# Optimization experiments

Hardware: AMD Instinct MI355X
Metric: run time of the kernel (lower is better)

The kernel has to match this reference:

```python
import jax, jax.numpy as jnp
import numpy as np

EMBED_DIM = 1024
NUM_HEADS = 16
HEAD_DIM = EMBED_DIM // NUM_HEADS
B, S = 2, 2048


def setup_inputs() -> dict:
    key = jax.random.key(0)
    ks = jax.random.split(key, 11)
    sc = 1.0 / np.sqrt(EMBED_DIM)
    d = {
        'query': jax.random.normal(ks[0], (B, S, EMBED_DIM), jnp.float32),
        'key': jax.random.normal(ks[1], (B, S, EMBED_DIM), jnp.float32),
        'value': jax.random.normal(ks[2], (B, S, EMBED_DIM), jnp.float32),
        'Wq': jax.random.normal(ks[3], (EMBED_DIM, EMBED_DIM), jnp.float32) * sc,
        'bq': jnp.zeros((EMBED_DIM,), jnp.float32),
        'Wk': jax.random.normal(ks[4], (EMBED_DIM, EMBED_DIM), jnp.float32) * sc,
        'bk': jnp.zeros((EMBED_DIM,), jnp.float32),
        'Wv': jax.random.normal(ks[5], (EMBED_DIM, EMBED_DIM), jnp.float32) * sc,
        'bv': jnp.zeros((EMBED_DIM,), jnp.float32),
        'Wo': jax.random.normal(ks[6], (EMBED_DIM, EMBED_DIM), jnp.float32) * sc,
        'bo': jnp.zeros((EMBED_DIM,), jnp.float32),
    }
    return d


def reference(query, key, value, Wq, bq, Wk, bk, Wv, bv, Wo, bo):
    b, s, _ = query.shape
    scale = 1.0 / np.sqrt(HEAD_DIM)
    # projections: torch Linear is x @ W.T + b
    q = (query @ Wq.T + bq).reshape(b, s, NUM_HEADS, HEAD_DIM).transpose(0, 2, 1, 3)
    k = (key @ Wk.T + bk).reshape(b, s, NUM_HEADS, HEAD_DIM).transpose(0, 2, 1, 3)
    v = (value @ Wv.T + bv).reshape(b, s, NUM_HEADS, HEAD_DIM).transpose(0, 2, 1, 3)
    scores = jnp.einsum('bhqd,bhkd->bhqk', q, k) * scale  # [B,H,S,S]
    causal = jnp.triu(jnp.ones((s, s), bool), k=1)
    scores = jnp.where(causal, -jnp.inf, scores)
    attn = jax.nn.softmax(scores, axis=-1)
    out = jnp.einsum('bhqk,bhkd->bhqd', attn, v)
    out = out.transpose(0, 2, 1, 3).reshape(b, s, EMBED_DIM)
    out = out @ Wo.T + bo
    return out, attn
```

## Files before the change

kernel.cpp:

```cpp
#include <hip/hip_runtime.h>
#include <hip/hip_bf16.h>

#define BATCH  2
#define SEQ    2048
#define EMBED  1024
#define NHEADS 16
#define HDIM   64
#define SCALE  0.125f
#define S2     0.180336880f
#define MFIX   20.0f
#define PPITCH 72

typedef __attribute__((ext_vector_type(8))) short   short8;
typedef __attribute__((ext_vector_type(4))) float   floatx4;

#if __has_builtin(__builtin_amdgcn_exp2f)
#define EXP2(x) __builtin_amdgcn_exp2f(x)
#else
#define EXP2(x) exp2f(x)
#endif

#define GLOAD_LDS(g, l) __builtin_amdgcn_global_load_lds(                      \
    (const __attribute__((address_space(1))) void*)(const void*)(g),           \
    (__attribute__((address_space(3))) void*)(void*)(l), 16, 0, 0)

__device__ __forceinline__ float bf2f(unsigned short h) {
    union { unsigned int u; float f; } v; v.u = ((unsigned int)h) << 16; return v.f;
}
__device__ __forceinline__ unsigned short f2bf(float f) {
    union { float f; unsigned int u; } v; v.f = f;
    unsigned int r = v.u + 0x7FFF + ((v.u >> 16) & 1);
    return (unsigned short)(r >> 16);
}
__device__ __forceinline__ unsigned int pack2(float lo, float hi) {
    return (unsigned int)f2bf(lo) | ((unsigned int)f2bf(hi) << 16);
}

__device__ __forceinline__ void bar_lds() {
    __builtin_amdgcn_sched_barrier(0);
    asm volatile("s_waitcnt lgkmcnt(0)" ::: "memory");
    __builtin_amdgcn_s_barrier();
    __builtin_amdgcn_sched_barrier(0);
}

__global__ __launch_bounds__(256)
void cvt_bf16(const float* __restrict__ q,  const float* __restrict__ k,
              const float* __restrict__ v,  const float* __restrict__ wq,
              const float* __restrict__ wk, const float* __restrict__ wv,
              const float* __restrict__ wo,
              unsigned short* __restrict__ dq,  unsigned short* __restrict__ dk,
              unsigned short* __restrict__ dv,  unsigned short* __restrict__ dwq,
              unsigned short* __restrict__ dwk, unsigned short* __restrict__ dwv,
              unsigned short* __restrict__ dwo)
{
    const float* s; unsigned short* d; int n;
    switch (blockIdx.y) {
        case 0: s = q;  d = dq;  n = BATCH * SEQ * EMBED; break;
        case 1: s = k;  d = dk;  n = BATCH * SEQ * EMBED; break;
        case 2: s = v;  d = dv;  n = BATCH * SEQ * EMBED; break;
        case 3: s = wq; d = dwq; n = EMBED * EMBED; break;
        case 4: s = wk; d = dwk; n = EMBED * EMBED; break;
        case 5: s = wv; d = dwv; n = EMBED * EMBED; break;
        default: s = wo; d = dwo; n = EMBED * EMBED; break;
    }
    const int i = (blockIdx.x * 256 + threadIdx.x) * 8;
    if (i >= n) return;
    float4 f0 = ((const float4*)(s + i))[0];
    float4 f1 = ((const float4*)(s + i))[1];
    uint4 u = {pack2(f0.x, f0.y), pack2(f0.z, f0.w),
               pack2(f1.x, f1.y), pack2(f1.z, f1.w)};
    *(uint4*)(d + i) = u;
}

__device__ __forceinline__ void gemm_body(
    const unsigned short* __restrict__ A,
    const unsigned short* __restrict__ W,
    const float* __restrict__ bias,
    void* __restrict__ Cout, const int f32out,
    const int bx, const int by)
{
    constexpr int N = EMBED;
    constexpr int K = EMBED;

    __shared__ unsigned short As[128 * 64];
    __shared__ unsigned short Bs[128 * 64];

    const int t    = threadIdx.x;
    const int w    = t >> 6;
    const int lane = t & 63;
    const int lr   = lane & 15;
    const int quad = lane >> 4;
    const int wr   = w >> 1;
    const int wc   = w & 1;
    const int n0   = bx * 128;
    const int m0   = by * 128;

    size_t agoff[4], bgoff[4];
    #pragma unroll
    for (int i = 0; i < 4; ++i) {
        const int slot = i * 256 + t;
        const int row  = slot >> 3;
        const int g    = (slot & 7) ^ (row & 7);
        agoff[i] = (size_t)(m0 + row) * K + g * 8;
        bgoff[i] = (size_t)(n0 + row) * K + g * 8;
    }

    int aoff[4][2], boff[4][2];
    #pragma unroll
    for (int mb = 0; mb < 4; ++mb)
        #pragma unroll
        for (int s = 0; s < 2; ++s) {
            const int row = wr * 64 + mb * 16 + lr;
            aoff[mb][s] = row * 64 + (((s * 4 + quad) ^ (row & 7)) * 8);
        }
    #pragma unroll
    for (int nb = 0; nb < 4; ++nb)
        #pragma unroll
        for (int s = 0; s < 2; ++s) {
            const int row = wc * 64 + nb * 16 + lr;
            boff[nb][s] = row * 64 + (((s * 4 + quad) ^ (row & 7)) * 8);
        }

    floatx4 acc[4][4];
    #pragma unroll
    for (int mb = 0; mb < 4; ++mb)
        #pragma unroll
        for (int nb = 0; nb < 4; ++nb) acc[mb][nb] = (floatx4){0.f, 0.f, 0.f, 0.f};

    for (int k0 = 0; k0 < K; k0 += 64) {
        __syncthreads();
        #pragma unroll
        for (int i = 0; i < 4; ++i)
            GLOAD_LDS(A + agoff[i] + k0, &As[(i * 256 + w * 64) * 8]);
        #pragma unroll
        for (int i = 0; i < 4; ++i)
            GLOAD_LDS(W + bgoff[i] + k0, &Bs[(i * 256 + w * 64) * 8]);
        __syncthreads();

        #pragma unroll
        for (int s = 0; s < 2; ++s) {
            short8 av[4], bv[4];
            #pragma unroll
            for (int mb = 0; mb < 4; ++mb) av[mb] = *(const short8*)&As[aoff[mb][s]];
            #pragma unroll
            for (int nb = 0; nb < 4; ++nb) bv[nb] = *(const short8*)&Bs[boff[nb][s]];
            #pragma unroll
            for (int mb = 0; mb < 4; ++mb)
                #pragma unroll
                for (int nb = 0; nb < 4; ++nb)
                    acc[mb][nb] = __builtin_amdgcn_mfma_f32_16x16x32_bf16(av[mb], bv[nb], acc[mb][nb], 0, 0, 0);
        }
    }

    #pragma unroll
    for (int mb = 0; mb < 4; ++mb)
        #pragma unroll
        for (int nb = 0; nb < 4; ++nb) {
            const int col = n0 + wc * 64 + nb * 16 + lr;
            const float bv = bias[col];
            #pragma unroll
            for (int r = 0; r < 4; ++r) {
                const int row = m0 + wr * 64 + mb * 16 + quad * 4 + r;
                const float val = acc[mb][nb][r] + bv;
                if (f32out) ((float*)Cout)[(size_t)row * N + col] = val;
                else        ((unsigned short*)Cout)[(size_t)row * N + col] = f2bf(val);
            }
        }
}

__global__ __launch_bounds__(256)
void gemm_qkv(const unsigned short* __restrict__ xq, const unsigned short* __restrict__ xk,
              const unsigned short* __restrict__ xv,
              const unsigned short* __restrict__ wq, const unsigned short* __restrict__ wk,
              const unsigned short* __restrict__ wv,
              const float* __restrict__ bq, const float* __restrict__ bk,
              const float* __restrict__ bv,
              unsigned short* __restrict__ Qb, unsigned short* __restrict__ Kb,
              unsigned short* __restrict__ Vb)
{
    const unsigned short *A, *W; const float* bias; unsigned short* C;
    switch (blockIdx.z) {
        case 0:  A = xq; W = wq; bias = bq; C = Qb; break;
        case 1:  A = xk; W = wk; bias = bk; C = Kb; break;
        default: A = xv; W = wv; bias = bv; C = Vb; break;
    }
    gemm_body(A, W, bias, C, 0, blockIdx.x, blockIdx.y);
}

__global__ __launch_bounds__(256)
void gemm_out(const unsigned short* __restrict__ A, const unsigned short* __restrict__ W,
              const float* __restrict__ bias, float* __restrict__ Cout)
{
    gemm_body(A, W, bias, Cout, 1, blockIdx.x, blockIdx.y);
}

__global__ __launch_bounds__(256)
void attn_pass(const unsigned short* __restrict__ Qb,
               const unsigned short* __restrict__ Kb,
               const unsigned short* __restrict__ Vb,
               float* __restrict__ attn,
               unsigned short* __restrict__ AO)
{
    __shared__ unsigned short Ks[2][64][PPITCH];
    __shared__ unsigned short Vt[2][64][PPITCH];
    __shared__ unsigned short Ps[64][PPITCH];

    const int t    = threadIdx.x;
    const int w    = t >> 6;
    const int lane = t & 63;
    const int lr   = lane & 15;
    const int quad = lane >> 4;
    const int h    = blockIdx.y;
    const int b    = blockIdx.z;
    const int slot = (h >> 3) + 2 * b;
    const int qt   = (slot & 1) ? (SEQ / 64 - 1 - (int)blockIdx.x) : (int)blockIdx.x;
    const int q0   = qt * 64;
    const int srow = t >> 2;
    const int sseg = (t & 3) * 16;
    const int bh   = b * NHEADS + h;

    const size_t kvbase = (size_t)b * SEQ * EMBED + h * HDIM;

    const unsigned short* qrow = Qb + kvbase + (size_t)(q0 + w * 16 + lr) * EMBED + quad * 8;
    const short8 af0 = *(const short8*)(qrow);
    const short8 af1 = *(const short8*)(qrow + 32);

    const unsigned short* Krow = Kb + kvbase + (size_t)srow * EMBED + sseg;
    const unsigned short* Vrow = Vb + kvbase + (size_t)lane * EMBED;

    uint4 kA0, kA1, vA0, vA1;
    uint4 kB0, kB1, vB0, vB1;

    kA0 = ((const uint4*)Krow)[0];
    kA1 = ((const uint4*)Krow)[1];
    vA0 = *(const uint4*)(Vrow + w * 8);
    vA1 = *(const uint4*)(Vrow + (w + 4) * 8);
    *(uint4*)&Ks[0][srow][sseg]     = kA0;
    *(uint4*)&Ks[0][srow][sseg + 8] = kA1;
    {
        const unsigned short* p0 = (const unsigned short*)&vA0;
        const unsigned short* p1 = (const unsigned short*)&vA1;
        #pragma unroll
        for (int j = 0; j < 8; ++j) Vt[0][w * 8 + j][lane]       = p0[j];
        #pragma unroll
        for (int j = 0; j < 8; ++j) Vt[0][(w + 4) * 8 + j][lane] = p1[j];
    }
    if (qt > 0) {
        const unsigned short* kp = Krow + (size_t)64 * EMBED;
        kB0 = ((const uint4*)kp)[0];
        kB1 = ((const uint4*)kp)[1];
        vB0 = *(const uint4*)(Vrow + (size_t)64 * EMBED + w * 8);
        vB1 = *(const uint4*)(Vrow + (size_t)64 * EMBED + (w + 4) * 8);
    }
    bar_lds();

    float lsum[4];
    #pragma unroll
    for (int r = 0; r < 4; ++r) lsum[r] = 0.f;
    floatx4 of[4];
    #pragma unroll
    for (int i = 0; i < 4; ++i) of[i] = (floatx4){0.f, 0.f, 0.f, 0.f};

    for (int kt = 0; kt <= qt; ++kt) {
        const int c  = kt & 1;
        const int k0 = kt * 64;

        if (kt < qt) {
            if ((kt & 1) == 0) {
                *(uint4*)&Ks[c ^ 1][srow][sseg]     = kB0;
                *(uint4*)&Ks[c ^ 1][srow][sseg + 8] = kB1;
                const unsigned short* p0 = (const unsigned short*)&vB0;
                const unsigned short* p1 = (const unsigned short*)&vB1;
                #pragma unroll
                for (int j = 0; j < 8; ++j) Vt[c ^ 1][w * 8 + j][lane]       = p0[j];
                #pragma unroll
                for (int j = 0; j < 8; ++j) Vt[c ^ 1][(w + 4) * 8 + j][lane] = p1[j];
                if (kt + 2 <= qt) {
                    const unsigned short* kp = Krow + (size_t)(k0 + 128) * EMBED;
                    kA0 = ((const uint4*)kp)[0];
                    kA1 = ((const uint4*)kp)[1];
                    vA0 = *(const uint4*)(Vrow + (size_t)(k0 + 128) * EMBED + w * 8);
                    vA1 = *(const uint4*)(Vrow + (size_t)(k0 + 128) * EMBED + (w + 4) * 8);
                }
            } else {
                *(uint4*)&Ks[c ^ 1][srow][sseg]     = kA0;
                *(uint4*)&Ks[c ^ 1][srow][sseg + 8] = kA1;
                const unsigned short* p0 = (const unsigned short*)&vA0;
                const unsigned short* p1 = (const unsigned short*)&vA1;
                #pragma unroll
                for (int j = 0; j < 8; ++j) Vt[c ^ 1][w * 8 + j][lane]       = p0[j];
                #pragma unroll
                for (int j = 0; j < 8; ++j) Vt[c ^ 1][(w + 4) * 8 + j][lane] = p1[j];
                if (kt + 2 <= qt) {
                    const unsigned short* kp = Krow + (size_t)(k0 + 128) * EMBED;
                    kB0 = ((const uint4*)kp)[0];
                    kB1 = ((const uint4*)kp)[1];
                    vB0 = *(const uint4*)(Vrow + (size_t)(k0 + 128) * EMBED + w * 8);
                    vB1 = *(const uint4*)(Vrow + (size_t)(k0 + 128) * EMBED + (w + 4) * 8);
                }
            }
        }

        floatx4 sf[4];
        #pragma unroll
        for (int i = 0; i < 4; ++i) sf[i] = (floatx4){0.f, 0.f, 0.f, 0.f};
        #pragma unroll
        for (int nb = 0; nb < 4; ++nb) {
            short8 bf0 = *(const short8*)&Ks[c][nb * 16 + lr][quad * 8];
            sf[nb] = __builtin_amdgcn_mfma_f32_16x16x32_bf16(af0, bf0, sf[nb], 0, 0, 0);
        }
        #pragma unroll
        for (int nb = 0; nb < 4; ++nb) {
            short8 bf1 = *(const short8*)&Ks[c][nb * 16 + lr][32 + quad * 8];
            sf[nb] = __builtin_amdgcn_mfma_f32_16x16x32_bf16(af1, bf1, sf[nb], 0, 0, 0);
        }

        if (kt < qt) {
            #pragma unroll
            for (int nb = 0; nb < 4; ++nb)
                #pragma unroll
                for (int r = 0; r < 4; ++r) {
                    float p = EXP2(sf[nb][r] * S2 - MFIX);
                    lsum[r] += p;
                    Ps[w * 16 + quad * 4 + r][nb * 16 + lr] = f2bf(p);
                }
        } else {
            #pragma unroll
            for (int nb = 0; nb < 4; ++nb) {
                const int k = nb * 16 + lr;
                #pragma unroll
                for (int r = 0; r < 4; ++r) {
                    const int q = w * 16 + quad * 4 + r;
                    float p = 0.f;
                    if (k <= q) { p = EXP2(sf[nb][r] * S2 - MFIX); lsum[r] += p; }
                    Ps[w * 16 + quad * 4 + r][nb * 16 + lr] = f2bf(p);
                }
            }
        }

        #pragma unroll
        for (int ss = 0; ss < 2; ++ss) {
            short8 paf = *(const short8*)&Ps[w * 16 + lr][ss * 32 + quad * 8];
            #pragma unroll
            for (int nb = 0; nb < 4; ++nb) {
                short8 vf = *(const short8*)&Vt[c][nb * 16 + lr][ss * 32 + quad * 8];
                of[nb] = __builtin_amdgcn_mfma_f32_16x16x32_bf16(paf, vf, of[nb], 0, 0, 0);
            }
        }

        bar_lds();
    }

    float invl[4];
    #pragma unroll
    for (int r = 0; r < 4; ++r) {
        #pragma unroll
        for (int off = 1; off < 16; off <<= 1)
            lsum[r] += __shfl_xor(lsum[r], off, 64);
        invl[r] = 1.f / lsum[r];
    }

    #pragma unroll
    for (int nb = 0; nb < 4; ++nb)
        #pragma unroll
        for (int r = 0; r < 4; ++r)
            Ps[w * 16 + quad * 4 + r][nb * 16 + lr] = f2bf(of[nb][r] * invl[r]);
    {
        const int rrow = lane >> 2;
        const int rseg = (lane & 3) * 16;
        unsigned short* ao = AO + (size_t)(b * SEQ + q0 + w * 16 + rrow) * EMBED + h * HDIM + rseg;
        *(uint4*)ao       = *(const uint4*)&Ps[w * 16 + rrow][rseg];
        *(uint4*)(ao + 8) = *(const uint4*)&Ps[w * 16 + rrow][rseg + 8];
    }

    kA0 = ((const uint4*)Krow)[0];
    kA1 = ((const uint4*)Krow)[1];
    if (qt > 0) {
        const unsigned short* kp = Krow + (size_t)64 * EMBED;
        kB0 = ((const uint4*)kp)[0];
        kB1 = ((const uint4*)kp)[1];
    }
    *(uint4*)&Ks[0][srow][sseg]     = kA0;
    *(uint4*)&Ks[0][srow][sseg + 8] = kA1;
    bar_lds();

    float* fb = attn + (size_t)bh * SEQ * SEQ;
    for (int kt = 0; kt <= qt; ++kt) {
        const int c  = kt & 1;
        const int k0 = kt * 64;

        if (kt < qt) {
            if ((kt & 1) == 0) {
                *(uint4*)&Ks[c ^ 1][srow][sseg]     = kB0;
                *(uint4*)&Ks[c ^ 1][srow][sseg + 8] = kB1;
                if (kt + 2 <= qt) {
                    const unsigned short* kp = Krow + (size_t)(k0 + 128) * EMBED;
                    kA0 = ((const uint4*)kp)[0];
                    kA1 = ((const uint4*)kp)[1];
                }
            } else {
                *(uint4*)&Ks[c ^ 1][srow][sseg]     = kA0;
                *(uint4*)&Ks[c ^ 1][srow][sseg + 8] = kA1;
                if (kt + 2 <= qt) {
                    const unsigned short* kp = Krow + (size_t)(k0 + 128) * EMBED;
                    kB0 = ((const uint4*)kp)[0];
                    kB1 = ((const uint4*)kp)[1];
                }
            }
        }

        floatx4 sf[4];
        #pragma unroll
        for (int i = 0; i < 4; ++i) sf[i] = (floatx4){0.f, 0.f, 0.f, 0.f};
        #pragma unroll
        for (int nb = 0; nb < 4; ++nb) {
            short8 bf0 = *(const short8*)&Ks[c][nb * 16 + lr][quad * 8];
            sf[nb] = __builtin_amdgcn_mfma_f32_16x16x32_bf16(af0, bf0, sf[nb], 0, 0, 0);
        }
        #pragma unroll
        for (int nb = 0; nb < 4; ++nb) {
            short8 bf1 = *(const short8*)&Ks[c][nb * 16 + lr][32 + quad * 8];
            sf[nb] = __builtin_amdgcn_mfma_f32_16x16x32_bf16(af1, bf1, sf[nb], 0, 0, 0);
        }

        float* frow = fb + (size_t)(q0 + w * 16 + quad * 4) * SEQ + k0;
        if (kt < qt) {
            #pragma unroll
            for (int nb = 0; nb < 4; ++nb)
                #pragma unroll
                for (int r = 0; r < 4; ++r)
                    frow[(size_t)r * SEQ + nb * 16 + lr] =
                        EXP2(sf[nb][r] * S2 - MFIX) * invl[r];
        } else {
            #pragma unroll
            for (int nb = 0; nb < 4; ++nb) {
                const int k = nb * 16 + lr;
                #pragma unroll
                for (int r = 0; r < 4; ++r) {
                    const int q = w * 16 + quad * 4 + r;
                    if (k <= q)
                        frow[(size_t)r * SEQ + nb * 16 + lr] =
                            EXP2(sf[nb][r] * S2 - MFIX) * invl[r];
                }
            }
        }

        bar_lds();
    }
}

extern "C" void kernel_launch(void* const* d_in, const int* in_sizes, int n_in,
                              void* d_out, int out_size, void* d_ws, size_t ws_size,
                              hipStream_t stream)
{
    const float* query = (const float*)d_in[0];
    const float* key   = (const float*)d_in[1];
    const float* value = (const float*)d_in[2];
    const float* Wq    = (const float*)d_in[3];
    const float* bq    = (const float*)d_in[4];
    const float* Wk    = (const float*)d_in[5];
    const float* bk    = (const float*)d_in[6];
    const float* Wv    = (const float*)d_in[7];
    const float* bv    = (const float*)d_in[8];
    const float* Wo    = (const float*)d_in[9];
    const float* bo    = (const float*)d_in[10];

    float* out  = (float*)d_out;
    float* attn = out + (size_t)BATCH * SEQ * EMBED;

    const size_t tsz = (size_t)BATCH * SEQ * EMBED;
    const size_t wsz = (size_t)EMBED * EMBED;
    unsigned short* p = (unsigned short*)d_ws;
    unsigned short* xq  = p;  p += tsz;
    unsigned short* xk  = p;  p += tsz;
    unsigned short* xv  = p;  p += tsz;
    unsigned short* wq16 = p; p += wsz;
    unsigned short* wk16 = p; p += wsz;
    unsigned short* wv16 = p; p += wsz;
    unsigned short* wo16 = p; p += wsz;
    unsigned short* Qb  = p;  p += tsz;
    unsigned short* Kb  = p;  p += tsz;
    unsigned short* Vb  = p;  p += tsz;
    unsigned short* AO  = p;  p += tsz;

    const dim3 blk(256);

    cvt_bf16<<<dim3(2048, 7), blk, 0, stream>>>(query, key, value, Wq, Wk, Wv, Wo,
                                                xq, xk, xv, wq16, wk16, wv16, wo16);

    const dim3 gqkv(EMBED / 128, (BATCH * SEQ) / 128, 3);
    gemm_qkv<<<gqkv, blk, 0, stream>>>(xq, xk, xv, wq16, wk16, wv16,
                                       bq, bk, bv, Qb, Kb, Vb);

    attn_pass<<<dim3(SEQ / 64, NHEADS, BATCH), blk, 0, stream>>>(
        Qb, Kb, Vb, attn, AO);

    gemm_out<<<dim3(EMBED / 128, (BATCH * SEQ) / 128), blk, 0, stream>>>(AO, wo16, bo, out);
}
```

Before: 721.0 us.

## Split attention-probability write into a second pass co-scheduled with output projection

The attention kernel now stops after computing the output and stores each row's inverse softmax denominator to a scratch buffer, which reuses the converted-query workspace. A new fused launch runs the output-projection GEMM blocks next to 1024 blocks that recompute QK^T and write the normalized fp32 attention matrix using the stored denominators. The goal is to take the large attention-matrix store off the attention kernel's critical path and overlap it with the projection GEMM. The cost is computing QK^T twice, and the store now depends on Lbuf and the row max being consistent between the two passes.

```diff
diff --git a/kernel.cpp b/kernel.cpp
--- a/kernel.cpp
+++ b/kernel.cpp
@@ -13,6 +13,7 @@
 
 typedef __attribute__((ext_vector_type(8))) short   short8;
 typedef __attribute__((ext_vector_type(4))) float   floatx4;
+typedef unsigned short ush;
 
 #if __has_builtin(__builtin_amdgcn_exp2f)
 #define EXP2(x) __builtin_amdgcn_exp2f(x)
@@ -24,13 +25,13 @@
     (const __attribute__((address_space(1))) void*)(const void*)(g),           \
     (__attribute__((address_space(3))) void*)(void*)(l), 16, 0, 0)
 
-__device__ __forceinline__ float bf2f(unsigned short h) {
+__device__ __forceinline__ float bf2f(ush h) {
     union { unsigned int u; float f; } v; v.u = ((unsigned int)h) << 16; return v.f;
 }
-__device__ __forceinline__ unsigned short f2bf(float f) {
+__device__ __forceinline__ ush f2bf(float f) {
     union { float f; unsigned int u; } v; v.f = f;
     unsigned int r = v.u + 0x7FFF + ((v.u >> 16) & 1);
-    return (unsigned short)(r >> 16);
+    return (ush)(r >> 16);
 }
 __device__ __forceinline__ unsigned int pack2(float lo, float hi) {
     return (unsigned int)f2bf(lo) | ((unsigned int)f2bf(hi) << 16);
@@ -48,12 +49,12 @@
               const float* __restrict__ v,  const float* __restrict__ wq,
               const float* __restrict__ wk, const float* __restrict__ wv,
               const float* __restrict__ wo,
-              unsigned short* __restrict__ dq,  unsigned short* __restrict__ dk,
-              unsigned short* __restrict__ dv,  unsigned short* __restrict__ dwq,
-              unsigned short* __restrict__ dwk, unsigned short* __restrict__ dwv,
-              unsigned short* __restrict__ dwo)
+              ush* __restrict__ dq,  ush* __restrict__ dk,
+              ush* __restrict__ dv,  ush* __restrict__ dwq,
+              ush* __restrict__ dwk, ush* __restrict__ dwv,
+              ush* __restrict__ dwo)
 {
-    const float* s; unsigned short* d; int n;
+    const float* s; ush* d; int n;
     switch (blockIdx.y) {
         case 0: s = q;  d = dq;  n = BATCH * SEQ * EMBED; break;
         case 1: s = k;  d = dk;  n = BATCH * SEQ * EMBED; break;
@@ -73,8 +74,9 @@
 }
 
 __device__ __forceinline__ void gemm_body(
-    const unsigned short* __restrict__ A,
-    const unsigned short* __restrict__ W,
+    char* smem,
+    const ush* __restrict__ A,
+    const ush* __restrict__ W,
     const float* __restrict__ bias,
     void* __restrict__ Cout, const int f32out,
     const int bx, const int by)
@@ -82,8 +84,8 @@
     constexpr int N = EMBED;
     constexpr int K = EMBED;
 
-    __shared__ unsigned short As[128 * 64];
-    __shared__ unsigned short Bs[128 * 64];
+    ush* As = (ush*)smem;
+    ush* Bs = (ush*)smem + 128 * 64;
 
     const int t    = threadIdx.x;
     const int w    = t >> 6;
@@ -163,47 +165,41 @@
                 const int row = m0 + wr * 64 + mb * 16 + quad * 4 + r;
                 const float val = acc[mb][nb][r] + bv;
                 if (f32out) ((float*)Cout)[(size_t)row * N + col] = val;
-                else        ((unsigned short*)Cout)[(size_t)row * N + col] = f2bf(val);
+                else        ((ush*)Cout)[(size_t)row * N + col] = f2bf(val);
             }
         }
 }
 
 __global__ __launch_bounds__(256)
-void gemm_qkv(const unsigned short* __restrict__ xq, const unsigned short* __restrict__ xk,
-              const unsigned short* __restrict__ xv,
-              const unsigned short* __restrict__ wq, const unsigned short* __restrict__ wk,
-              const unsigned short* __restrict__ wv,
+void gemm_qkv(const ush* __restrict__ xq, const ush* __restrict__ xk,
+              const ush* __restrict__ xv,
+              const ush* __restrict__ wq, const ush* __restrict__ wk,
+              const ush* __restrict__ wv,
               const float* __restrict__ bq, const float* __restrict__ bk,
               const float* __restrict__ bv,
-              unsigned short* __restrict__ Qb, unsigned short* __restrict__ Kb,
-              unsigned short* __restrict__ Vb)
+              ush* __restrict__ Qb, ush* __restrict__ Kb,
+              ush* __restrict__ Vb)
 {
-    const unsigned short *A, *W; const float* bias; unsigned short* C;
+    __shared__ __align__(16) char smem[32768];
+    const ush *A, *W; const float* bias; ush* C;
     switch (blockIdx.z) {
         case 0:  A = xq; W = wq; bias = bq; C = Qb; break;
         case 1:  A = xk; W = wk; bias = bk; C = Kb; break;
         default: A = xv; W = wv; bias = bv; C = Vb; break;
     }
-    gemm_body(A, W, bias, C, 0, blockIdx.x, blockIdx.y);
+    gemm_body(smem, A, W, bias, C, 0, blockIdx.x, blockIdx.y);
 }
 
 __global__ __launch_bounds__(256)
-void gemm_out(const unsigned short* __restrict__ A, const unsigned short* __restrict__ W,
-              const float* __restrict__ bias, float* __restrict__ Cout)
+void attn_pass(const ush* __restrict__ Qb,
+               const ush* __restrict__ Kb,
+               const ush* __restrict__ Vb,
+               float* __restrict__ Lbuf,
+               ush* __restrict__ AO)
 {
-    gemm_body(A, W, bias, Cout, 1, blockIdx.x, blockIdx.y);
-}
-
-__global__ __launch_bounds__(256)
-void attn_pass(const unsigned short* __restrict__ Qb,
-               const unsigned short* __restrict__ Kb,
-               const unsigned short* __restrict__ Vb,
-               float* __restrict__ attn,
-               unsigned short* __restrict__ AO)
-{
-    __shared__ unsigned short Ks[2][64][PPITCH];
-    __shared__ unsigned short Vt[2][64][PPITCH];
-    __shared__ unsigned short Ps[64][PPITCH];
+    __shared__ ush Ks[2][64][PPITCH];
+    __shared__ ush Vt[2][64][PPITCH];
+    __shared__ ush Ps[64][PPITCH];
 
     const int t    = threadIdx.x;
     const int w    = t >> 6;
@@ -221,12 +217,12 @@
 
     const size_t kvbase = (size_t)b * SEQ * EMBED + h * HDIM;
 
-    const unsigned short* qrow = Qb + kvbase + (size_t)(q0 + w * 16 + lr) * EMBED + quad * 8;
+    const ush* qrow = Qb + kvbase + (size_t)(q0 + w * 16 + lr) * EMBED + quad * 8;
     const short8 af0 = *(const short8*)(qrow);
     const short8 af1 = *(const short8*)(qrow + 32);
 
-    const unsigned short* Krow = Kb + kvbase + (size_t)srow * EMBED + sseg;
-    const unsigned short* Vrow = Vb + kvbase + (size_t)lane * EMBED;
+    const ush* Krow = Kb + kvbase + (size_t)srow * EMBED + sseg;
+    const ush* Vrow = Vb + kvbase + (size_t)lane * EMBED;
 
     uint4 kA0, kA1, vA0, vA1;
     uint4 kB0, kB1, vB0, vB1;
@@ -238,15 +234,15 @@
     *(uint4*)&Ks[0][srow][sseg]     = kA0;
     *(uint4*)&Ks[0][srow][sseg + 8] = kA1;
     {
-        const unsigned short* p0 = (const unsigned short*)&vA0;
-        const unsigned short* p1 = (const unsigned short*)&vA1;
+        const ush* p0 = (const ush*)&vA0;
+        const ush* p1 = (const ush*)&vA1;
         #pragma unroll
         for (int j = 0; j < 8; ++j) Vt[0][w * 8 + j][lane]       = p0[j];
         #pragma unroll
         for (int j = 0; j < 8; ++j) Vt[0][(w + 4) * 8 + j][lane] = p1[j];
     }
     if (qt > 0) {
-        const unsigned short* kp = Krow + (size_t)64 * EMBED;
+        const ush* kp = Krow + (size_t)64 * EMBED;
         kB0 = ((const uint4*)kp)[0];
         kB1 = ((const uint4*)kp)[1];
         vB0 = *(const uint4*)(Vrow + (size_t)64 * EMBED + w * 8);
@@ -269,14 +265,14 @@
             if ((kt & 1) == 0) {
                 *(uint4*)&Ks[c ^ 1][srow][sseg]     = kB0;
                 *(uint4*)&Ks[c ^ 1][srow][sseg + 8] = kB1;
-                const unsigned short* p0 = (const unsigned short*)&vB0;
-                const unsigned short* p1 = (const unsigned short*)&vB1;
+                const ush* p0 = (const ush*)&vB0;
+                const ush* p1 = (const ush*)&vB1;
                 #pragma unroll
                 for (int j = 0; j < 8; ++j) Vt[c ^ 1][w * 8 + j][lane]       = p0[j];
                 #pragma unroll
                 for (int j = 0; j < 8; ++j) Vt[c ^ 1][(w + 4) * 8 + j][lane] = p1[j];
                 if (kt + 2 <= qt) {
-                    const unsigned short* kp = Krow + (size_t)(k0 + 128) * EMBED;
+                    const ush* kp = Krow + (size_t)(k0 + 128) * EMBED;
                     kA0 = ((const uint4*)kp)[0];
                     kA1 = ((const uint4*)kp)[1];
                     vA0 = *(const uint4*)(Vrow + (size_t)(k0 + 128) * EMBED + w * 8);
@@ -285,14 +281,14 @@
             } else {
                 *(uint4*)&Ks[c ^ 1][srow][sseg]     = kA0;
                 *(uint4*)&Ks[c ^ 1][srow][sseg + 8] = kA1;
-                const unsigned short* p0 = (const unsigned short*)&vA0;
-                const unsigned short* p1 = (const unsigned short*)&vA1;
+                const ush* p0 = (const ush*)&vA0;
+                const ush* p1 = (const ush*)&vA1;
                 #pragma unroll
                 for (int j = 0; j < 8; ++j) Vt[c ^ 1][w * 8 + j][lane]       = p0[j];
                 #pragma unroll
                 for (int j = 0; j < 8; ++j) Vt[c ^ 1][(w + 4) * 8 + j][lane] = p1[j];
                 if (kt + 2 <= qt) {
-                    const unsigned short* kp = Krow + (size_t)(k0 + 128) * EMBED;
+                    const ush* kp = Krow + (size_t)(k0 + 128) * EMBED;
                     kB0 = ((const uint4*)kp)[0];
                     kB1 = ((const uint4*)kp)[1];
                     vB0 = *(const uint4*)(Vrow + (size_t)(k0 + 128) * EMBED + w * 8);
@@ -359,6 +355,11 @@
             lsum[r] += __shfl_xor(lsum[r], off, 64);
         invl[r] = 1.f / lsum[r];
     }
+    if (lr == 0) {
+        #pragma unroll
+        for (int r = 0; r < 4; ++r)
+            Lbuf[(size_t)bh * SEQ + q0 + w * 16 + quad * 4 + r] = invl[r];
+    }
 
     #pragma unroll
     for (int nb = 0; nb < 4; ++nb)
@@ -368,15 +369,63 @@
     {
         const int rrow = lane >> 2;
         const int rseg = (lane & 3) * 16;
-        unsigned short* ao = AO + (size_t)(b * SEQ + q0 + w * 16 + rrow) * EMBED + h * HDIM + rseg;
+        ush* ao = AO + (size_t)(b * SEQ + q0 + w * 16 + rrow) * EMBED + h * HDIM + rseg;
         *(uint4*)ao       = *(const uint4*)&Ps[w * 16 + rrow][rseg];
         *(uint4*)(ao + 8) = *(const uint4*)&Ps[w * 16 + rrow][rseg + 8];
     }
-
+}
+
+__global__ __launch_bounds__(256)
+void gemm_out_norm(const ush* __restrict__ AO, const ush* __restrict__ Wo16,
+                   const float* __restrict__ bo, float* __restrict__ out,
+                   const ush* __restrict__ Qb, const ush* __restrict__ Kb,
+                   float* __restrict__ attn, const float* __restrict__ Lbuf)
+{
+    __shared__ __align__(16) char smem[32768];
+
+    const int id = blockIdx.x;
+    if (id < 256) {
+        gemm_body(smem, AO, Wo16, bo, out, 1, id & 7, id >> 3);
+        return;
+    }
+
+    ush (*Ks)[64][PPITCH] = (ush(*)[64][PPITCH])smem;
+
+    const int id2  = id - 256;
+    const int bh   = id2 >> 5;
+    const int x    = id2 & 31;
+    const int b    = bh >> 4;
+    const int h    = bh & 15;
+    const int slot = (h >> 3) + 2 * b;
+    const int qt   = (slot & 1) ? (SEQ / 64 - 1 - x) : x;
+    const int q0   = qt * 64;
+
+    const int t    = threadIdx.x;
+    const int w    = t >> 6;
+    const int lane = t & 63;
+    const int lr   = lane & 15;
+    const int quad = lane >> 4;
+    const int srow = t >> 2;
+    const int sseg = (t & 3) * 16;
+
+    const size_t kvbase = (size_t)b * SEQ * EMBED + h * HDIM;
+
+    const ush* qrow = Qb + kvbase + (size_t)(q0 + w * 16 + lr) * EMBED + quad * 8;
+    const short8 af0 = *(const short8*)(qrow);
+    const short8 af1 = *(const short8*)(qrow + 32);
+
+    float invl[4];
+    #pragma unroll
+    for (int r = 0; r < 4; ++r)
+        invl[r] = Lbuf[(size_t)bh * SEQ + q0 + w * 16 + quad * 4 + r];
+
+    const ush* Krow = Kb + kvbase + (size_t)srow * EMBED + sseg;
+
+    uint4 kA0, kA1, kB0, kB1;
     kA0 = ((const uint4*)Krow)[0];
     kA1 = ((const uint4*)Krow)[1];
     if (qt > 0) {
-        const unsigned short* kp = Krow + (size_t)64 * EMBED;
+        const ush* kp = Krow + (size_t)64 * EMBED;
         kB0 = ((const uint4*)kp)[0];
         kB1 = ((const uint4*)kp)[1];
     }
@@ -394,7 +443,7 @@
                 *(uint4*)&Ks[c ^ 1][srow][sseg]     = kB0;
                 *(uint4*)&Ks[c ^ 1][srow][sseg + 8] = kB1;
                 if (kt + 2 <= qt) {
-                    const unsigned short* kp = Krow + (size_t)(k0 + 128) * EMBED;
+                    const ush* kp = Krow + (size_t)(k0 + 128) * EMBED;
                     kA0 = ((const uint4*)kp)[0];
                     kA1 = ((const uint4*)kp)[1];
                 }
@@ -402,7 +451,7 @@
                 *(uint4*)&Ks[c ^ 1][srow][sseg]     = kA0;
                 *(uint4*)&Ks[c ^ 1][srow][sseg + 8] = kA1;
                 if (kt + 2 <= qt) {
-                    const unsigned short* kp = Krow + (size_t)(k0 + 128) * EMBED;
+                    const ush* kp = Krow + (size_t)(k0 + 128) * EMBED;
                     kB0 = ((const uint4*)kp)[0];
                     kB1 = ((const uint4*)kp)[1];
                 }
@@ -483,6 +532,8 @@
     unsigned short* Vb  = p;  p += tsz;
     unsigned short* AO  = p;  p += tsz;
 
+    float* Lbuf = (float*)xq;
+
     const dim3 blk(256);
 
     cvt_bf16<<<dim3(2048, 7), blk, 0, stream>>>(query, key, value, Wq, Wk, Wv, Wo,
@@ -493,7 +544,8 @@
                                        bq, bk, bv, Qb, Kb, Vb);
 
     attn_pass<<<dim3(SEQ / 64, NHEADS, BATCH), blk, 0, stream>>>(
-        Qb, Kb, Vb, attn, AO);
-
-    gemm_out<<<dim3(EMBED / 128, (BATCH * SEQ) / 128), blk, 0, stream>>>(AO, wo16, bo, out);
-}
+        Qb, Kb, Vb, Lbuf, AO);
+
+    gemm_out_norm<<<dim3(256 + 1024), blk, 0, stream>>>(
+        AO, wo16, bo, out, Qb, Kb, attn, Lbuf);
+}
```

After: 723.7 us. No clear change (+0.4%).
